# Optimization experiments

Hardware: AMD Instinct MI355X
Metric: run time of the kernel (lower is better)

Reference implementation:

```python
import jax, jax.numpy as jnp
import numpy as np

NUM_SUB = 2  # top-k experts kept by the gate


def setup_inputs() -> dict:
    key = jax.random.key(0)
    kx, kr, kw = jax.random.split(key, 3)
    B, C, H, W, E = 16, 256, 64, 64, 8
    inputs = jax.random.normal(kx, (B, C, H, W), dtype=jnp.float32)
    W_router = jax.random.normal(kr, (C, E), dtype=jnp.float32) / np.sqrt(C)
    b_router = jnp.zeros((E,), dtype=jnp.float32)
    W_exp = jax.random.normal(kw, (E, C, C), dtype=jnp.float32) / np.sqrt(C)
    b_exp = jnp.zeros((E, C), dtype=jnp.float32)
    return {"inputs": inputs, "W_router": W_router, "b_router": b_router,
            "W_exp": W_exp, "b_exp": b_exp, "k": 2}


def reference(inputs, W_router, b_router, W_exp, b_exp, k):
    # Router: global-avg-pool + linear -> [B, E]
    E = W_router.shape[1]
    pooled = inputs.mean(axis=(2, 3))                       # [B, C]
    logits = pooled @ W_router + b_router                   # [B, E]
    # softmax in fp32 then cast back (matches F.softmax(..., dtype=torch.float))
    weights = jax.nn.softmax(logits.astype(jnp.float32), axis=1).astype(inputs.dtype)
    # top-k gating: scatter of gathered values == weights * topk-mask
    _, topk_idx = jax.lax.top_k(weights, NUM_SUB)            # [B, k]
    mask = jax.nn.one_hot(topk_idx, E, dtype=weights.dtype).sum(axis=1)  # [B, E]
    exp_w = weights * mask                                   # sparse gates [B, E]
    # out = inputs + sum_e gate[b,e] * (conv1x1_e(inputs))
    # expert weight W_exp[e, d, c]: out_d = sum_c W[d,c] x_c + b_d
    out = inputs \
        + jnp.einsum('be,edc,bchw->bdhw', exp_w, W_exp, inputs) \
        + jnp.einsum('be,ed->bd', exp_w, b_exp)[:, :, None, None]
    return out
```

## Files before the change

### kernel.cpp

```cpp
#include <hip/hip_runtime.h>
#include <hip/hip_bf16.h>

typedef __bf16 bf16x8 __attribute__((ext_vector_type(8)));
typedef float f32x4 __attribute__((ext_vector_type(4)));
typedef unsigned short ushort4v __attribute__((ext_vector_type(4)));
typedef unsigned short ushort8v __attribute__((ext_vector_type(8)));

#define B_  16
#define C_  256
#define HW_ 4096
#define E_  8

__device__ inline unsigned short f2bf(float f) {
    unsigned int b = __builtin_bit_cast(unsigned int, f);
    b += 0x7FFFu + ((b >> 16) & 1u);
    return (unsigned short)(b >> 16);
}

__global__ __launch_bounds__(256) void k_pool(const float* __restrict__ in,
                                              float* __restrict__ pooled) {
    int bc = blockIdx.x;
    const float* p = in + (size_t)bc * HW_;
    int t = threadIdx.x;
    float s = 0.f;
#pragma unroll
    for (int i = 0; i < 4; i++) {
        float4 v = *reinterpret_cast<const float4*>(p + (size_t)(t + i * 256) * 4);
        s += v.x + v.y + v.z + v.w;
    }
#pragma unroll
    for (int off = 32; off; off >>= 1) s += __shfl_down(s, off, 64);
    __shared__ float part[4];
    if ((t & 63) == 0) part[t >> 6] = s;
    __syncthreads();
    if (t == 0) pooled[bc] = (part[0] + part[1] + part[2] + part[3]) * (1.0f / HW_);
}

__global__ __launch_bounds__(256) void k_wg(const float* __restrict__ pooled,
                                            const float* __restrict__ Wr,
                                            const float* __restrict__ br,
                                            const float* __restrict__ Wexp,
                                            const float* __restrict__ bexp,
                                            unsigned short* __restrict__ Weff,
                                            float* __restrict__ biasE) {
    __shared__ float pooledS[C_];
    __shared__ float wrs[C_ * E_];
    __shared__ float lgp[64];
    __shared__ float gL[E_];
    const int t = threadIdx.x;
    const int b = blockIdx.y, dblk = blockIdx.x;

    pooledS[t] = pooled[b * C_ + t];
#pragma unroll
    for (int i = 0; i < 2; ++i)
        reinterpret_cast<float4*>(wrs)[t + i * 256] =
            reinterpret_cast<const float4*>(Wr)[t + i * 256];
    __syncthreads();
    if (t < 64) {
        const int e = t & 7, seg = t >> 3;
        float s = 0.f;
#pragma unroll
        for (int c = seg * 32; c < seg * 32 + 32; ++c)
            s += pooledS[c] * wrs[c * E_ + e];
        lgp[t] = s;
    }
    __syncthreads();
    if (t == 0) {
        float w[E_];
        float m = -1e30f;
#pragma unroll
        for (int e = 0; e < E_; ++e) {
            float s = br[e];
#pragma unroll
            for (int k = 0; k < 8; ++k) s += lgp[k * 8 + e];
            w[e] = s; m = fmaxf(m, s);
        }
        float sum = 0.f;
#pragma unroll
        for (int e = 0; e < E_; ++e) { w[e] = __expf(w[e] - m); sum += w[e]; }
        float inv = 1.f / sum;
#pragma unroll
        for (int e = 0; e < E_; ++e) w[e] *= inv;
        int i0 = 0;
#pragma unroll
        for (int e = 1; e < E_; ++e) if (w[e] > w[i0]) i0 = e;
        int i1 = -1;
#pragma unroll
        for (int e = 0; e < E_; ++e) {
            if (e == i0) continue;
            if (i1 < 0 || w[e] > w[i1]) i1 = e;
        }
#pragma unroll
        for (int e = 0; e < E_; ++e)
            gL[e] = (e == i0 || e == i1) ? w[e] : 0.f;
    }
    __syncthreads();
    if (dblk == 0) {
        float s = 0.f;
#pragma unroll
        for (int e = 0; e < E_; ++e) s += gL[e] * bexp[e * C_ + t];
        biasE[b * C_ + t] = s;
    }
    const int dloc = t >> 5, cq = t & 31;
    const int d = dblk * 8 + dloc;
#pragma unroll
    for (int half = 0; half < 2; half++) {
        const int c = (cq + half * 32) * 4;
        float4 a = {0.f, 0.f, 0.f, 0.f};
#pragma unroll
        for (int e = 0; e < E_; e++) {
            float ge = gL[e];
            if (ge != 0.f) {
                float4 wv = *reinterpret_cast<const float4*>(
                    Wexp + ((size_t)(e * C_ + d)) * C_ + c);
                a.x += ge * wv.x; a.y += ge * wv.y;
                a.z += ge * wv.z; a.w += ge * wv.w;
            }
        }
        ushort4v o = { f2bf(a.x), f2bf(a.y), f2bf(a.z), f2bf(a.w) };
        *reinterpret_cast<ushort4v*>(Weff + ((size_t)(b * C_ + d)) * C_ + c) = o;
    }
}

__global__ __launch_bounds__(512, 8) void k_fused(const float* __restrict__ in,
                                                  const unsigned short* __restrict__ Weff,
                                                  const float* __restrict__ biasE,
                                                  float* __restrict__ out) {
    __shared__ unsigned short Bs[64 * 256];
    __shared__ unsigned int   TsU[32 * 33];
    __shared__ float biasS[C_];

    const int t  = threadIdx.x;
    const int b  = blockIdx.y;
    const int n0 = blockIdx.x * 64;
    const int lane = t & 63, w = t >> 6;
    const int kg = lane >> 4, lr = lane & 15;
    const float* Xb = in + ((size_t)b * C_) * HW_ + n0;
    const unsigned short* Ab = Weff + (size_t)b * C_ * C_;

    if (t < C_) biasS[t] = biasE[b * C_ + t];

    {
        const int cl = t >> 4;
        const int pq = (t & 15) * 4;
        const int pr = t & 63;
        const int c8 = t >> 6;
        for (int pass = 0; pass < 8; ++pass) {
            float4 v = *reinterpret_cast<const float4*>(
                Xb + (size_t)(pass * 32 + cl) * HW_ + pq);
            unsigned int* tr = &TsU[cl * 33 + (t & 15) * 2];
            tr[0] = (unsigned int)f2bf(v.x) | ((unsigned int)f2bf(v.y) << 16);
            tr[1] = (unsigned int)f2bf(v.z) | ((unsigned int)f2bf(v.w) << 16);
            __syncthreads();
            const int half = pr & 1;
            ushort4v u;
#pragma unroll
            for (int j = 0; j < 4; ++j) {
                unsigned int wv = TsU[(c8 * 4 + j) * 33 + (pr >> 1)];
                u[j] = (unsigned short)(half ? (wv >> 16) : (wv & 0xffff));
            }
            const int lc = pass * 4 + (c8 >> 1);
            const int cs = lc ^ (pr & 7);
            *reinterpret_cast<ushort4v*>(&Bs[pr * 256 + cs * 8 + (c8 & 1) * 4]) = u;
            __syncthreads();
        }
    }

    f32x4 acc[2][4];
#pragma unroll
    for (int mi = 0; mi < 2; ++mi) {
#pragma unroll
        for (int j = 0; j < 4; ++j) {
            const int row = w * 32 + mi * 16 + kg * 4 + j;
            const float bias = biasS[row];
#pragma unroll
            for (int ni = 0; ni < 4; ++ni) {
                const int p = ni * 16 + lr;
                unsigned short xv =
                    Bs[p * 256 + (((row >> 3) ^ (p & 7)) * 8) + (row & 7)];
                acc[mi][ni][j] =
                    __builtin_bit_cast(float, (unsigned int)xv << 16) + bias;
            }
        }
    }

#pragma unroll
    for (int kf = 0; kf < 8; ++kf) {
        bf16x8 af[2];
#pragma unroll
        for (int mi = 0; mi < 2; ++mi) {
            const int row = w * 32 + mi * 16 + lr;
            af[mi] = __builtin_bit_cast(bf16x8,
                *reinterpret_cast<const ushort8v*>(
                    &Ab[(size_t)row * C_ + kf * 32 + kg * 8]));
        }
#pragma unroll
        for (int ni = 0; ni < 4; ++ni) {
            const int p = ni * 16 + lr;
            const int cc = (kf * 4 + kg) ^ (p & 7);
            bf16x8 bfv = __builtin_bit_cast(bf16x8,
                *reinterpret_cast<const ushort8v*>(&Bs[p * 256 + cc * 8]));
            acc[0][ni] = __builtin_amdgcn_mfma_f32_16x16x32_bf16(
                af[0], bfv, acc[0][ni], 0, 0, 0);
            acc[1][ni] = __builtin_amdgcn_mfma_f32_16x16x32_bf16(
                af[1], bfv, acc[1][ni], 0, 0, 0);
        }
    }

    float* outB = out + ((size_t)b * C_) * HW_ + n0;
#pragma unroll
    for (int mi = 0; mi < 2; ++mi) {
#pragma unroll
        for (int j = 0; j < 4; ++j) {
            const int row = w * 32 + mi * 16 + kg * 4 + j;
            float* orow = outB + (size_t)row * HW_;
#pragma unroll
            for (int ni = 0; ni < 4; ++ni)
                orow[ni * 16 + lr] = acc[mi][ni][j];
        }
    }
}

extern "C" void kernel_launch(void* const* d_in, const int* in_sizes, int n_in,
                              void* d_out, int out_size, void* d_ws, size_t ws_size,
                              hipStream_t stream) {
    const float* in   = (const float*)d_in[0];
    const float* Wr   = (const float*)d_in[1];
    const float* br   = (const float*)d_in[2];
    const float* Wexp = (const float*)d_in[3];
    const float* bexp = (const float*)d_in[4];
    float* out = (float*)d_out;
    char* ws = (char*)d_ws;

    float* pooled         = (float*)(ws);
    float* biasE          = (float*)(ws + 0x11000);
    unsigned short* Weff  = (unsigned short*)(ws + 0x20000);

    hipLaunchKernelGGL(k_pool,  dim3(B_ * C_), dim3(256), 0, stream, in, pooled);
    hipLaunchKernelGGL(k_wg,    dim3(32, B_),  dim3(256), 0, stream,
                       pooled, Wr, br, Wexp, bexp, Weff, biasE);
    hipLaunchKernelGGL(k_fused, dim3(HW_ / 64, B_), dim3(512), 0, stream,
                       in, Weff, biasE, out);
}
```

Before: 53.71 us.

## Fuse pooling into a bf16 transpose pre-pass and stream tiles into LDS

```diff
diff --git a/kernel.cpp b/kernel.cpp
--- a/kernel.cpp
+++ b/kernel.cpp
@@ -17,26 +17,60 @@
     return (unsigned short)(b >> 16);
 }
 
-__global__ __launch_bounds__(256) void k_pool(const float* __restrict__ in,
-                                              float* __restrict__ pooled) {
-    int bc = blockIdx.x;
-    const float* p = in + (size_t)bc * HW_;
-    int t = threadIdx.x;
-    float s = 0.f;
-#pragma unroll
-    for (int i = 0; i < 4; i++) {
-        float4 v = *reinterpret_cast<const float4*>(p + (size_t)(t + i * 256) * 4);
-        s += v.x + v.y + v.z + v.w;
-    }
-#pragma unroll
-    for (int off = 32; off; off >>= 1) s += __shfl_down(s, off, 64);
-    __shared__ float part[4];
-    if ((t & 63) == 0) part[t >> 6] = s;
-    __syncthreads();
-    if (t == 0) pooled[bc] = (part[0] + part[1] + part[2] + part[3]) * (1.0f / HW_);
-}
-
-__global__ __launch_bounds__(256) void k_wg(const float* __restrict__ pooled,
+__global__ __launch_bounds__(512, 8) void k_prep(const float* __restrict__ in,
+                                                 float* __restrict__ partial,
+                                                 unsigned short* __restrict__ Xt) {
+    __shared__ unsigned short Bs[64 * 256];
+    __shared__ unsigned int   TsU[32 * 33];
+    const int t  = threadIdx.x;
+    const int pt = blockIdx.x;
+    const int b  = blockIdx.y;
+    const int p0 = pt * 64;
+    const float* Xb = in + ((size_t)b * C_) * HW_ + p0;
+    const int lane = t & 63;
+    const int cl = t >> 4;
+    const int pq = (t & 15) * 4;
+    const int pr = t & 63;
+    const int c8 = t >> 6;
+
+#pragma unroll
+    for (int pass = 0; pass < 8; ++pass) {
+        float4 v = *reinterpret_cast<const float4*>(
+            Xb + (size_t)(pass * 32 + cl) * HW_ + pq);
+        unsigned int* tr = &TsU[cl * 33 + (t & 15) * 2];
+        tr[0] = (unsigned int)f2bf(v.x) | ((unsigned int)f2bf(v.y) << 16);
+        tr[1] = (unsigned int)f2bf(v.z) | ((unsigned int)f2bf(v.w) << 16);
+        float s = v.x + v.y + v.z + v.w;
+        s += __shfl_xor(s, 1, 64);
+        s += __shfl_xor(s, 2, 64);
+        s += __shfl_xor(s, 4, 64);
+        s += __shfl_xor(s, 8, 64);
+        if ((lane & 15) == 0)
+            partial[(size_t)(b * C_ + pass * 32 + cl) * 64 + pt] = s;
+        __syncthreads();
+        const int half = pr & 1;
+        ushort4v u;
+#pragma unroll
+        for (int j = 0; j < 4; ++j) {
+            unsigned int wv = TsU[(c8 * 4 + j) * 33 + (pr >> 1)];
+            u[j] = (unsigned short)(half ? (wv >> 16) : (wv & 0xffff));
+        }
+        const int lc = pass * 4 + (c8 >> 1);
+        const int cs = lc ^ (pr & 7);
+        *reinterpret_cast<ushort4v*>(&Bs[pr * 256 + cs * 8 + (c8 & 1) * 4]) = u;
+        __syncthreads();
+    }
+
+    unsigned short* dst = Xt + ((size_t)(b * HW_ + p0)) * C_;
+#pragma unroll
+    for (int i = 0; i < 4; ++i) {
+        const int off = i * 4096 + t * 8;
+        *reinterpret_cast<ushort8v*>(dst + off) =
+            *reinterpret_cast<const ushort8v*>(Bs + off);
+    }
+}
+
+__global__ __launch_bounds__(256) void k_wg(const float* __restrict__ partial,
                                             const float* __restrict__ Wr,
                                             const float* __restrict__ br,
                                             const float* __restrict__ Wexp,
@@ -50,7 +84,17 @@
     const int t = threadIdx.x;
     const int b = blockIdx.y, dblk = blockIdx.x;
 
-    pooledS[t] = pooled[b * C_ + t];
+    {
+        const float4* p4 = reinterpret_cast<const float4*>(
+            partial + (size_t)(b * C_ + t) * 64);
+        float s = 0.f;
+#pragma unroll
+        for (int j = 0; j < 16; ++j) {
+            float4 v = p4[j];
+            s += v.x + v.y + v.z + v.w;
+        }
+        pooledS[t] = s * (1.0f / HW_);
+    }
 #pragma unroll
     for (int i = 0; i < 2; ++i)
         reinterpret_cast<float4*>(wrs)[t + i * 256] =
@@ -122,49 +166,32 @@
     }
 }
 
-__global__ __launch_bounds__(512, 8) void k_fused(const float* __restrict__ in,
-                                                  const unsigned short* __restrict__ Weff,
-                                                  const float* __restrict__ biasE,
-                                                  float* __restrict__ out) {
+__global__ __launch_bounds__(512, 8) void k_gemm(const unsigned short* __restrict__ Xt,
+                                                 const unsigned short* __restrict__ Weff,
+                                                 const float* __restrict__ biasE,
+                                                 float* __restrict__ out) {
     __shared__ unsigned short Bs[64 * 256];
-    __shared__ unsigned int   TsU[32 * 33];
     __shared__ float biasS[C_];
 
     const int t  = threadIdx.x;
+    const int pt = blockIdx.x;
     const int b  = blockIdx.y;
-    const int n0 = blockIdx.x * 64;
+    const int n0 = pt * 64;
     const int lane = t & 63, w = t >> 6;
     const int kg = lane >> 4, lr = lane & 15;
-    const float* Xb = in + ((size_t)b * C_) * HW_ + n0;
     const unsigned short* Ab = Weff + (size_t)b * C_ * C_;
+    const unsigned short* src = Xt + ((size_t)(b * HW_ + n0)) * C_;
 
     if (t < C_) biasS[t] = biasE[b * C_ + t];
 
-    {
-        const int cl = t >> 4;
-        const int pq = (t & 15) * 4;
-        const int pr = t & 63;
-        const int c8 = t >> 6;
-        for (int pass = 0; pass < 8; ++pass) {
-            float4 v = *reinterpret_cast<const float4*>(
-                Xb + (size_t)(pass * 32 + cl) * HW_ + pq);
-            unsigned int* tr = &TsU[cl * 33 + (t & 15) * 2];
-            tr[0] = (unsigned int)f2bf(v.x) | ((unsigned int)f2bf(v.y) << 16);
-            tr[1] = (unsigned int)f2bf(v.z) | ((unsigned int)f2bf(v.w) << 16);
-            __syncthreads();
-            const int half = pr & 1;
-            ushort4v u;
-#pragma unroll
-            for (int j = 0; j < 4; ++j) {
-                unsigned int wv = TsU[(c8 * 4 + j) * 33 + (pr >> 1)];
-                u[j] = (unsigned short)(half ? (wv >> 16) : (wv & 0xffff));
-            }
-            const int lc = pass * 4 + (c8 >> 1);
-            const int cs = lc ^ (pr & 7);
-            *reinterpret_cast<ushort4v*>(&Bs[pr * 256 + cs * 8 + (c8 & 1) * 4]) = u;
-            __syncthreads();
-        }
-    }
+#pragma unroll
+    for (int i = 0; i < 4; ++i) {
+        const int chunk = i * 8 + w;
+        __builtin_amdgcn_global_load_lds(
+            (const __attribute__((address_space(1))) void*)(src + chunk * 512 + lane * 8),
+            (__attribute__((address_space(3))) void*)(Bs + chunk * 512), 16, 0, 0);
+    }
+    __syncthreads();
 
     f32x4 acc[2][4];
 #pragma unroll
@@ -232,13 +259,14 @@
     float* out = (float*)d_out;
     char* ws = (char*)d_ws;
 
-    float* pooled         = (float*)(ws);
-    float* biasE          = (float*)(ws + 0x11000);
-    unsigned short* Weff  = (unsigned short*)(ws + 0x20000);
-
-    hipLaunchKernelGGL(k_pool,  dim3(B_ * C_), dim3(256), 0, stream, in, pooled);
-    hipLaunchKernelGGL(k_wg,    dim3(32, B_),  dim3(256), 0, stream,
-                       pooled, Wr, br, Wexp, bexp, Weff, biasE);
-    hipLaunchKernelGGL(k_fused, dim3(HW_ / 64, B_), dim3(512), 0, stream,
-                       in, Weff, biasE, out);
-}
+    float* partial        = (float*)(ws);
+    unsigned short* Xt    = (unsigned short*)(ws + 0x100000);
+    unsigned short* Weff  = (unsigned short*)(ws + 0x2100000);
+    float* biasE          = (float*)(ws + 0x2300000);
+
+    hipLaunchKernelGGL(k_prep, dim3(64, B_), dim3(512), 0, stream, in, partial, Xt);
+    hipLaunchKernelGGL(k_wg,   dim3(32, B_), dim3(256), 0, stream,
+                       partial, Wr, br, Wexp, bexp, Weff, biasE);
+    hipLaunchKernelGGL(k_gemm, dim3(64, B_), dim3(512), 0, stream,
+                       Xt, Weff, biasE, out);
+}
```

Result: slower. 57.20 us (+6.5%).

## Fold residual identity into Weff and swap MFMA operands for vector stores

Applied to the files above, without the earlier changes.

```diff
diff --git a/kernel.cpp b/kernel.cpp
--- a/kernel.cpp
+++ b/kernel.cpp
@@ -117,6 +117,11 @@
                 a.z += ge * wv.z; a.w += ge * wv.w;
             }
         }
+        const int diff = d - c;
+        if (diff == 0) a.x += 1.f;
+        else if (diff == 1) a.y += 1.f;
+        else if (diff == 2) a.z += 1.f;
+        else if (diff == 3) a.w += 1.f;
         ushort4v o = { f2bf(a.x), f2bf(a.y), f2bf(a.z), f2bf(a.w) };
         *reinterpret_cast<ushort4v*>(Weff + ((size_t)(b * C_ + d)) * C_ + c) = o;
     }
@@ -168,55 +173,44 @@
 
     f32x4 acc[2][4];
 #pragma unroll
-    for (int mi = 0; mi < 2; ++mi) {
-#pragma unroll
-        for (int j = 0; j < 4; ++j) {
-            const int row = w * 32 + mi * 16 + kg * 4 + j;
-            const float bias = biasS[row];
-#pragma unroll
-            for (int ni = 0; ni < 4; ++ni) {
-                const int p = ni * 16 + lr;
-                unsigned short xv =
-                    Bs[p * 256 + (((row >> 3) ^ (p & 7)) * 8) + (row & 7)];
-                acc[mi][ni][j] =
-                    __builtin_bit_cast(float, (unsigned int)xv << 16) + bias;
-            }
-        }
+    for (int fd = 0; fd < 2; ++fd) {
+        const float bias = biasS[w * 32 + fd * 16 + lr];
+#pragma unroll
+        for (int pf = 0; pf < 4; ++pf)
+            acc[fd][pf] = (f32x4){bias, bias, bias, bias};
     }
 
 #pragma unroll
     for (int kf = 0; kf < 8; ++kf) {
-        bf16x8 af[2];
-#pragma unroll
-        for (int mi = 0; mi < 2; ++mi) {
-            const int row = w * 32 + mi * 16 + lr;
-            af[mi] = __builtin_bit_cast(bf16x8,
+        bf16x8 wf[2];
+#pragma unroll
+        for (int fd = 0; fd < 2; ++fd) {
+            const int row = w * 32 + fd * 16 + lr;
+            wf[fd] = __builtin_bit_cast(bf16x8,
                 *reinterpret_cast<const ushort8v*>(
                     &Ab[(size_t)row * C_ + kf * 32 + kg * 8]));
         }
 #pragma unroll
-        for (int ni = 0; ni < 4; ++ni) {
-            const int p = ni * 16 + lr;
+        for (int pf = 0; pf < 4; ++pf) {
+            const int p = pf * 16 + lr;
             const int cc = (kf * 4 + kg) ^ (p & 7);
-            bf16x8 bfv = __builtin_bit_cast(bf16x8,
+            bf16x8 xf = __builtin_bit_cast(bf16x8,
                 *reinterpret_cast<const ushort8v*>(&Bs[p * 256 + cc * 8]));
-            acc[0][ni] = __builtin_amdgcn_mfma_f32_16x16x32_bf16(
-                af[0], bfv, acc[0][ni], 0, 0, 0);
-            acc[1][ni] = __builtin_amdgcn_mfma_f32_16x16x32_bf16(
-                af[1], bfv, acc[1][ni], 0, 0, 0);
+            acc[0][pf] = __builtin_amdgcn_mfma_f32_16x16x32_bf16(
+                xf, wf[0], acc[0][pf], 0, 0, 0);
+            acc[1][pf] = __builtin_amdgcn_mfma_f32_16x16x32_bf16(
+                xf, wf[1], acc[1][pf], 0, 0, 0);
         }
     }
 
     float* outB = out + ((size_t)b * C_) * HW_ + n0;
 #pragma unroll
-    for (int mi = 0; mi < 2; ++mi) {
-#pragma unroll
-        for (int j = 0; j < 4; ++j) {
-            const int row = w * 32 + mi * 16 + kg * 4 + j;
-            float* orow = outB + (size_t)row * HW_;
-#pragma unroll
-            for (int ni = 0; ni < 4; ++ni)
-                orow[ni * 16 + lr] = acc[mi][ni][j];
+    for (int fd = 0; fd < 2; ++fd) {
+        const int row = w * 32 + fd * 16 + lr;
+        float* orow = outB + (size_t)row * HW_;
+#pragma unroll
+        for (int pf = 0; pf < 4; ++pf) {
+            *reinterpret_cast<f32x4*>(&orow[pf * 16 + kg * 4]) = acc[fd][pf];
         }
     }
 }
```

Result: no change. 54.32 us (+1.1%).
